# Kernel optimization log

Hardware: AMD Instinct MI355X
Metric: run time of the kernel (lower is better)

## Reference

```python
import jax, jax.numpy as jnp
import numpy as np


def _grid_sample_bilinear(img, grid):
    # img: [B,C,H,W]; grid: [B,Hg,Wg,2] normalized to [-1,1] (x,y), align_corners=False,
    # zero padding (torch F.grid_sample defaults).
    B, C, H, W = img.shape
    Hg, Wg = grid.shape[1], grid.shape[2]
    gx, gy = grid[..., 0], grid[..., 1]
    ix = (gx + 1.0) * (W * 0.5) - 0.5
    iy = (gy + 1.0) * (H * 0.5) - 0.5
    ix0 = jnp.floor(ix)
    iy0 = jnp.floor(iy)
    tx = (ix - ix0).reshape(B, 1, -1)
    ty = (iy - iy0).reshape(B, 1, -1)
    img_flat = img.reshape(B, C, H * W)

    def corner(xi, yi):
        valid = ((xi >= 0) & (xi < W) & (yi >= 0) & (yi < H)).reshape(B, 1, -1)
        xc = jnp.clip(xi, 0, W - 1).astype(jnp.int32)
        yc = jnp.clip(yi, 0, H - 1).astype(jnp.int32)
        idx = (yc * W + xc).reshape(B, -1)                      # [B, Hg*Wg]
        vals = jax.vmap(lambda f, i: f[:, i])(img_flat, idx)    # [B, C, Hg*Wg]
        return vals * valid

    v00 = corner(ix0, iy0)
    v01 = corner(ix0 + 1, iy0)
    v10 = corner(ix0, iy0 + 1)
    v11 = corner(ix0 + 1, iy0 + 1)
    out = (v00 * (1 - tx) * (1 - ty) + v01 * tx * (1 - ty)
           + v10 * (1 - tx) * ty + v11 * tx * ty)
    return out.reshape(B, C, Hg, Wg)


def setup_inputs() -> dict:
    key = jax.random.key(0)
    ks = jax.random.split(key, 8)
    B, C, RHO, WP = 32, 384, 25, 256
    HC, WC = 64, 64
    D = 2 * C  # 768, channels after polar/cart concat
    std = 0.02
    return {
        "polar_feat": jax.random.normal(ks[0], (B, C, RHO, WP), jnp.float32),
        "cart_feat": jax.random.normal(ks[1], (B, C, HC, WC), jnp.float32),
        "grid": jax.random.uniform(ks[2], (B, RHO, WP, 2), jnp.float32, -1.0, 1.0),
        "W1_0": jax.random.normal(ks[3], (D, 40), jnp.float32) * std,
        "b1_0": jnp.zeros((40,), jnp.float32),
        "W2_0": jax.random.normal(ks[4], (40, 1), jnp.float32) * std,
        "b2_0": jnp.zeros((1,), jnp.float32),
        "W1s": jax.random.normal(ks[5], (24, D + 1, 40), jnp.float32) * std,
        "b1s": jnp.zeros((24, 40), jnp.float32),
        "W2s": jax.random.normal(ks[6], (24, 40, 1), jnp.float32) * std,
        "b2s": jnp.zeros((24, 1), jnp.float32),
    }


def reference(polar_feat, cart_feat, grid, W1_0, b1_0, W2_0, b2_0, W1s, b1s, W2s, b2s):
    # Polar grid-sample fusion of cartesian features onto the polar grid.
    fe_cart_p = _grid_sample_bilinear(cart_feat, grid)              # [B,C,25,Wp]
    fe_cat_p = jnp.concatenate([polar_feat, fe_cart_p], axis=1)     # [B,768,25,Wp]
    # AdaptiveAvgPool2d((None,1)): mean over width.
    fe = jnp.mean(fe_cat_p, axis=3)                                 # [B,768,25]

    feats = jnp.transpose(fe, (2, 0, 1))                            # [25,B,768]
    gelu = lambda x: jax.nn.gelu(x, approximate=False)

    # Head 0: no recurrent input.
    h0 = gelu(feats[0] @ W1_0 + b1_0)
    out0 = h0 @ W2_0 + b2_0                                         # [B,1]

    # Heads 1..24: concat previous scalar output before first linear (fully_local=False).
    def step(out_prev, xs):
        feat, W1, b1, W2, b2 = xs
        x = jnp.concatenate([feat, out_prev], axis=-1)              # [B,769]
        h = gelu(x @ W1 + b1)
        o = h @ W2 + b2                                             # [B,1]
        return o, o

    _, outs = jax.lax.scan(step, out0, (feats[1:], W1s, b1s, W2s, b2s))
    out = jnp.concatenate([out0[None], outs], axis=0)               # [25,B,1]
    out = jnp.transpose(out[:, :, 0], (1, 0))                       # [B,25]
    return jnp.clip(out, 0.0, jnp.pi)
```

## Files before the change

kernel.cpp:

```cpp
#include <hip/hip_runtime.h>
#include <math.h>

#define B_    32
#define C_    384
#define RHO_  25
#define WP_   256
#define PIX_  4096
#define D_    768
#define HID_  40
#define NROWS (B_*C_*RHO_)
#define FE_N (RHO_*B_*D_)
#define POLARBLK 2048
#define PCH 8

typedef _Float16 half_t;
typedef __attribute__((ext_vector_type(8))) _Float16 half8;
typedef __attribute__((ext_vector_type(4))) float f32x4;

__device__ __forceinline__ float gelu_exact(float x) {
    return 0.5f * x * (1.f + erff(x * 0.70710678118654752f));
}

__global__ __launch_bounds__(256) void front_kernel(const float* __restrict__ polar,
        const float* __restrict__ grid,
        const float* __restrict__ W1_0, const float* __restrict__ W1s,
        half_t* __restrict__ Whi, half_t* __restrict__ Wlo,
        float* __restrict__ W1T, float* __restrict__ fe) {
    __shared__ float lb[PIX_];
    int tid = threadIdx.x;
    int bid = blockIdx.x;
    if (bid < POLARBLK) {
        int wid = bid * 4 + (tid >> 6);
        int lane = tid & 63;
        const int NW = POLARBLK * 4;
        for (int r0 = wid; r0 < NROWS; r0 += 4 * NW) {
            float s[4];
            #pragma unroll
            for (int k = 0; k < 4; ++k) {
                int r = r0 + k * NW;
                float4 v = (r < NROWS) ? ((const float4*)(polar + (size_t)r * WP_))[lane]
                                       : make_float4(0.f, 0.f, 0.f, 0.f);
                s[k] = v.x + v.y + v.z + v.w;
            }
            #pragma unroll
            for (int m = 32; m >= 1; m >>= 1) {
                #pragma unroll
                for (int k = 0; k < 4; ++k) s[k] += __shfl_xor(s[k], m, 64);
            }
            if (lane == 0) {
                #pragma unroll
                for (int k = 0; k < 4; ++k) {
                    int r = r0 + k * NW;
                    if (r < NROWS) {
                        int rho = r % RHO_, cch = (r / RHO_) % C_, bb = r / (RHO_ * C_);
                        fe[((size_t)(rho * B_ + bb)) * D_ + cch] = s[k] * (1.f / 256.f);
                    }
                }
            }
        }
    } else if (bid < POLARBLK + B_ * RHO_) {
        int bb = bid - POLARBLK;
        for (int i = tid; i < PIX_ / 4; i += 256) ((float4*)lb)[i] = make_float4(0.f, 0.f, 0.f, 0.f);
        __syncthreads();
        int pt = bb * WP_ + tid;
        float2 g = ((const float2*)grid)[pt];
        float ix = (g.x + 1.f) * 32.f - 0.5f;
        float iy = (g.y + 1.f) * 32.f - 0.5f;
        float x0f = floorf(ix), y0f = floorf(iy);
        float fx = ix - x0f, fy = iy - y0f;
        int x0 = (int)x0f, y0 = (int)y0f;
        const float s = 1.f / 256.f;
        if ((unsigned)x0 < 64u) {
            if ((unsigned)y0 < 64u)       atomicAdd(&lb[y0 * 64 + x0],       (1.f - fx) * (1.f - fy) * s);
            if ((unsigned)(y0 + 1) < 64u) atomicAdd(&lb[(y0 + 1) * 64 + x0], (1.f - fx) * fy * s);
        }
        if ((unsigned)(x0 + 1) < 64u) {
            if ((unsigned)y0 < 64u)       atomicAdd(&lb[y0 * 64 + x0 + 1],       fx * (1.f - fy) * s);
            if ((unsigned)(y0 + 1) < 64u) atomicAdd(&lb[(y0 + 1) * 64 + x0 + 1], fx * fy * s);
        }
        __syncthreads();
        int b = bb / RHO_, rho = bb % RHO_;
        half_t* wh = Whi + ((size_t)(b * 32 + rho)) * PIX_;
        half_t* wl = Wlo + ((size_t)(b * 32 + rho)) * PIX_;
        for (int i = tid; i < PIX_; i += 256) {
            float wv = lb[i];
            half_t h = (half_t)wv;
            wh[i] = h;
            wl[i] = (half_t)(wv - (float)h);
        }
    } else if (bid < POLARBLK + B_ * RHO_ + 25) {
        int i = bid - (POLARBLK + B_ * RHO_);
        const float* src = (i == 0) ? W1_0 : (W1s + (size_t)(i - 1) * 769 * HID_);
        float* dst = W1T + (size_t)i * HID_ * D_;
        for (int idx = tid; idx < HID_ * D_; idx += 256) {
            int j = idx / D_, c = idx % D_;
            dst[idx] = src[c * HID_ + j];
        }
    } else {
        int z = bid - (POLARBLK + B_ * RHO_ + 25);
        for (int i = tid; i < 16 * 96; i += 256) {
            int row = z * 16 + (i / 96), e = i % 96;
            ((float4*)fe)[(size_t)row * 192 + 96 + e] = make_float4(0.f, 0.f, 0.f, 0.f);
        }
    }
}

__global__ __launch_bounds__(256) void cart_mfma_kernel(const float* __restrict__ cart,
        const half_t* __restrict__ Whi, const half_t* __restrict__ Wlo,
        float* __restrict__ fe) {
    __shared__ float lds_out[1600];
    int tid = threadIdx.x;
    int bid = blockIdx.x;
    int b  = bid / (6 * PCH);
    int ct = (bid / PCH) % 6;
    int pc = bid % PCH;
    int w = tid >> 6, lane = tid & 63;
    int row16 = lane & 15, kg = lane >> 4;

    const float*  xrow = cart + ((size_t)b * C_ + ct * 64 + w * 16 + row16) * PIX_ + pc * 512 + kg * 8;
    const half_t* bh0 = Whi + ((size_t)(b * 32 + row16)) * PIX_ + pc * 512 + kg * 8;
    const half_t* bh1 = Whi + ((size_t)(b * 32 + 16 + row16)) * PIX_ + pc * 512 + kg * 8;
    const half_t* bl0 = Wlo + ((size_t)(b * 32 + row16)) * PIX_ + pc * 512 + kg * 8;
    const half_t* bl1 = Wlo + ((size_t)(b * 32 + 16 + row16)) * PIX_ + pc * 512 + kg * 8;

    f32x4 acc0 = {0.f, 0.f, 0.f, 0.f};
    f32x4 acc1 = {0.f, 0.f, 0.f, 0.f};

    float4 xa = *(const float4*)(xrow);
    float4 xb = *(const float4*)(xrow + 4);
    half8 nbh0 = *(const half8*)(bh0);
    half8 nbh1 = *(const half8*)(bh1);
    half8 nbl0 = *(const half8*)(bl0);
    half8 nbl1 = *(const half8*)(bl1);

    for (int t = 0; t < 16; ++t) {
        float4 cxa = xa, cxb = xb;
        half8 vbh0 = nbh0, vbh1 = nbh1, vbl0 = nbl0, vbl1 = nbl1;
        if (t < 15) {
            int off = (t + 1) * 32;
            xa = *(const float4*)(xrow + off);
            xb = *(const float4*)(xrow + off + 4);
            nbh0 = *(const half8*)(bh0 + off);
            nbh1 = *(const half8*)(bh1 + off);
            nbl0 = *(const half8*)(bl0 + off);
            nbl1 = *(const half8*)(bl1 + off);
        }
        float xs[8] = {cxa.x, cxa.y, cxa.z, cxa.w, cxb.x, cxb.y, cxb.z, cxb.w};
        half8 ah, al;
        #pragma unroll
        for (int i = 0; i < 8; ++i) {
            half_t h = (half_t)xs[i];
            ah[i] = h;
            al[i] = (half_t)(xs[i] - (float)h);
        }
        acc0 = __builtin_amdgcn_mfma_f32_16x16x32_f16(ah, vbh0, acc0, 0, 0, 0);
        acc0 = __builtin_amdgcn_mfma_f32_16x16x32_f16(ah, vbl0, acc0, 0, 0, 0);
        acc0 = __builtin_amdgcn_mfma_f32_16x16x32_f16(al, vbh0, acc0, 0, 0, 0);
        acc1 = __builtin_amdgcn_mfma_f32_16x16x32_f16(ah, vbh1, acc1, 0, 0, 0);
        acc1 = __builtin_amdgcn_mfma_f32_16x16x32_f16(ah, vbl1, acc1, 0, 0, 0);
        acc1 = __builtin_amdgcn_mfma_f32_16x16x32_f16(al, vbh1, acc1, 0, 0, 0);
    }

    #pragma unroll
    for (int r = 0; r < 4; ++r)
        lds_out[(lane & 15) * 64 + w * 16 + kg * 4 + r] = acc0[r];
    int rho1 = 16 + (lane & 15);
    if (rho1 < RHO_) {
        #pragma unroll
        for (int r = 0; r < 4; ++r)
            lds_out[rho1 * 64 + w * 16 + kg * 4 + r] = acc1[r];
    }
    __syncthreads();
    for (int oi = tid; oi < 1600; oi += 256) {
        int r = oi >> 6, cc = oi & 63;
        atomicAdd(&fe[((size_t)(r * B_ + b)) * D_ + 384 + ct * 64 + cc], lds_out[oi]);
    }
}

__global__ __launch_bounds__(256) void mlp_pre_kernel(const float* __restrict__ fe,
        const float* __restrict__ W1T, const float* __restrict__ b1_0,
        const float* __restrict__ b1s, float* __restrict__ G) {
    int lane = threadIdx.x & 63;
    int trip = blockIdx.x * 4 + (threadIdx.x >> 6);
    int jh = trip & 1;
    int pair = trip >> 1;
    int i = pair >> 5, b = pair & 31;
    const float4* f4p = (const float4*)(fe + (size_t)(i * B_ + b) * D_);
    float4 f0 = f4p[lane], f1 = f4p[lane + 64], f2 = f4p[lane + 128];
    int j0 = jh * 20;
    #pragma unroll 2
    for (int j = j0; j < j0 + 20; ++j) {
        const float4* w4p = (const float4*)(W1T + ((size_t)i * HID_ + j) * D_);
        float4 w0 = w4p[lane], w1 = w4p[lane + 64], w2 = w4p[lane + 128];
        float s = f0.x*w0.x + f0.y*w0.y + f0.z*w0.z + f0.w*w0.w
                + f1.x*w1.x + f1.y*w1.y + f1.z*w1.z + f1.w*w1.w
                + f2.x*w2.x + f2.y*w2.y + f2.z*w2.z + f2.w*w2.w;
        #pragma unroll
        for (int m = 32; m >= 1; m >>= 1) s += __shfl_xor(s, m, 64);
        if (lane == 0) {
            float bias = (i == 0) ? b1_0[j] : b1s[(i - 1) * HID_ + j];
            G[(size_t)(i * B_ + b) * HID_ + j] = s + bias;
        }
    }
}

__global__ __launch_bounds__(64) void mlp_seq_kernel(const float* __restrict__ G,
        const float* __restrict__ W1s, const float* __restrict__ W2_0,
        const float* __restrict__ b2_0, const float* __restrict__ W2s,
        const float* __restrict__ b2s, float* __restrict__ out) {
    int lane = threadIdx.x;
    int j2 = lane & 31, b = blockIdx.x * 2 + (lane >> 5);
    bool hi = (j2 < 8);
    float g1[25], g2[25], wl1[25], wl2[25], w2a[25], w2b[25], bsc[25];
    #pragma unroll
    for (int i = 0; i < 25; ++i) {
        g1[i] = G[(size_t)(i * B_ + b) * HID_ + j2];
        g2[i] = hi ? G[(size_t)(i * B_ + b) * HID_ + 32 + j2] : 0.f;
    }
    wl1[0] = 0.f; wl2[0] = 0.f;
    w2a[0] = W2_0[j2]; w2b[0] = hi ? W2_0[32 + j2] : 0.f; bsc[0] = b2_0[0];
    #pragma unroll
    for (int i = 1; i < 25; ++i) {
        size_t base = ((size_t)(i - 1) * 769 + 768) * HID_;
        wl1[i] = W1s[base + j2];
        wl2[i] = hi ? W1s[base + 32 + j2] : 0.f;
        w2a[i] = W2s[(i - 1) * HID_ + j2];
        w2b[i] = hi ? W2s[(i - 1) * HID_ + 32 + j2] : 0.f;
        bsc[i] = b2s[i - 1];
    }
    float op = 0.f;
    #pragma unroll
    for (int i = 0; i < 25; ++i) {
        float x1 = g1[i] + op * wl1[i];
        float x2 = g2[i] + op * wl2[i];
        float p = gelu_exact(x1) * w2a[i] + gelu_exact(x2) * w2b[i];
        #pragma unroll
        for (int m = 16; m >= 1; m >>= 1) p += __shfl_xor(p, m, 64);
        float o = p + bsc[i];
        op = o;
        if (j2 == 0) out[b * 25 + i] = fminf(fmaxf(o, 0.f), 3.14159265358979323846f);
    }
}

extern "C" void kernel_launch(void* const* d_in, const int* in_sizes, int n_in,
                              void* d_out, int out_size, void* d_ws, size_t ws_size,
                              hipStream_t stream) {
    const float* polar = (const float*)d_in[0];
    const float* cart  = (const float*)d_in[1];
    const float* grid  = (const float*)d_in[2];
    const float* W1_0  = (const float*)d_in[3];
    const float* b1_0  = (const float*)d_in[4];
    const float* W2_0  = (const float*)d_in[5];
    const float* b2_0  = (const float*)d_in[6];
    const float* W1s   = (const float*)d_in[7];
    const float* b1s   = (const float*)d_in[8];
    const float* W2s   = (const float*)d_in[9];
    const float* b2s   = (const float*)d_in[10];
    float* out = (float*)d_out;

    half_t* Whi = (half_t*)d_ws;
    half_t* Wlo = Whi + (size_t)B_ * 32 * PIX_;
    float* fe   = (float*)(Wlo + (size_t)B_ * 32 * PIX_);
    float* G    = fe + (size_t)FE_N;
    float* W1T  = G + (size_t)RHO_ * B_ * HID_;

    front_kernel<<<POLARBLK + B_ * RHO_ + 25 + 50, 256, 0, stream>>>(polar, grid, W1_0, W1s, Whi, Wlo, W1T, fe);
    cart_mfma_kernel<<<B_ * 6 * PCH, 256, 0, stream>>>(cart, Whi, Wlo, fe);
    mlp_pre_kernel<<<(RHO_ * B_ * 2) / 4, 256, 0, stream>>>(fe, W1T, b1_0, b1s, G);
    mlp_seq_kernel<<<B_ / 2, 64, 0, stream>>>(G, W1s, W2_0, b2_0, W2s, b2s, out);
}
```

Baseline: 198.3 us.

## Stage cart rows through per-wave LDS double buffer for coalesced loads

The cart-feature GEMM kernel no longer has each lane read its own strided 32-byte pieces of global memory. Each wave now loads 64-column tiles of its 16 rows with row-contiguous float4 reads, writes them into a padded, double-buffered per-wave LDS area, and reads the MFMA A fragments back from LDS. Weight fragments are prefetched two K-steps ahead in registers. This is meant to improve global load coalescing and hide latency, at the cost of about 34KB of LDS per block (lower occupancy), more registers, and LDS traffic. It relies on wave-local ordering with no barrier between the LDS writes and reads.

Result: faster. 175.4 us (-11.5%).

```diff
diff --git a/kernel.cpp b/kernel.cpp
--- a/kernel.cpp
+++ b/kernel.cpp
@@ -108,7 +108,7 @@
 __global__ __launch_bounds__(256) void cart_mfma_kernel(const float* __restrict__ cart,
         const half_t* __restrict__ Whi, const half_t* __restrict__ Wlo,
         float* __restrict__ fe) {
-    __shared__ float lds_out[1600];
+    __shared__ float smem[8704];
     int tid = threadIdx.x;
     int bid = blockIdx.x;
     int b  = bid / (6 * PCH);
@@ -117,63 +117,102 @@
     int w = tid >> 6, lane = tid & 63;
     int row16 = lane & 15, kg = lane >> 4;
 
-    const float*  xrow = cart + ((size_t)b * C_ + ct * 64 + w * 16 + row16) * PIX_ + pc * 512 + kg * 8;
+    const float* xgbase = cart + ((size_t)b * C_ + ct * 64 + w * 16) * PIX_ + pc * 512;
     const half_t* bh0 = Whi + ((size_t)(b * 32 + row16)) * PIX_ + pc * 512 + kg * 8;
-    const half_t* bh1 = Whi + ((size_t)(b * 32 + 16 + row16)) * PIX_ + pc * 512 + kg * 8;
+    const half_t* bh1 = bh0 + (size_t)16 * PIX_;
     const half_t* bl0 = Wlo + ((size_t)(b * 32 + row16)) * PIX_ + pc * 512 + kg * 8;
-    const half_t* bl1 = Wlo + ((size_t)(b * 32 + 16 + row16)) * PIX_ + pc * 512 + kg * 8;
+    const half_t* bl1 = bl0 + (size_t)16 * PIX_;
+
+    float* xl = smem + w * 2176;
+    int srow = lane >> 4;
+    int scol = (lane & 15) * 4;
 
     f32x4 acc0 = {0.f, 0.f, 0.f, 0.f};
     f32x4 acc1 = {0.f, 0.f, 0.f, 0.f};
-
-    float4 xa = *(const float4*)(xrow);
-    float4 xb = *(const float4*)(xrow + 4);
-    half8 nbh0 = *(const half8*)(bh0);
-    half8 nbh1 = *(const half8*)(bh1);
-    half8 nbl0 = *(const half8*)(bl0);
-    half8 nbl1 = *(const half8*)(bl1);
-
-    for (int t = 0; t < 16; ++t) {
-        float4 cxa = xa, cxb = xb;
-        half8 vbh0 = nbh0, vbh1 = nbh1, vbl0 = nbl0, vbl1 = nbl1;
-        if (t < 15) {
-            int off = (t + 1) * 32;
-            xa = *(const float4*)(xrow + off);
-            xb = *(const float4*)(xrow + off + 4);
-            nbh0 = *(const half8*)(bh0 + off);
-            nbh1 = *(const half8*)(bh1 + off);
-            nbl0 = *(const half8*)(bl0 + off);
-            nbl1 = *(const half8*)(bl1 + off);
-        }
-        float xs[8] = {cxa.x, cxa.y, cxa.z, cxa.w, cxb.x, cxb.y, cxb.z, cxb.w};
-        half8 ah, al;
+    float4 sreg[4];
+    half8 wf[2][8];
+
+    #pragma unroll
+    for (int i = 0; i < 4; ++i)
+        sreg[i] = *(const float4*)(xgbase + (size_t)(srow + 4 * i) * PIX_ + scol);
+    #pragma unroll
+    for (int ks = 0; ks < 2; ++ks) {
+        wf[0][ks * 4 + 0] = *(const half8*)(bh0 + ks * 32);
+        wf[0][ks * 4 + 1] = *(const half8*)(bh1 + ks * 32);
+        wf[0][ks * 4 + 2] = *(const half8*)(bl0 + ks * 32);
+        wf[0][ks * 4 + 3] = *(const half8*)(bl1 + ks * 32);
+    }
+    #pragma unroll
+    for (int i = 0; i < 4; ++i)
+        *(float4*)(&xl[(srow + 4 * i) * 68 + scol]) = sreg[i];
+    #pragma unroll
+    for (int i = 0; i < 4; ++i)
+        sreg[i] = *(const float4*)(xgbase + (size_t)(srow + 4 * i) * PIX_ + 64 + scol);
+    #pragma unroll
+    for (int ks = 0; ks < 2; ++ks) {
+        wf[1][ks * 4 + 0] = *(const half8*)(bh0 + 64 + ks * 32);
+        wf[1][ks * 4 + 1] = *(const half8*)(bh1 + 64 + ks * 32);
+        wf[1][ks * 4 + 2] = *(const half8*)(bl0 + 64 + ks * 32);
+        wf[1][ks * 4 + 3] = *(const half8*)(bl1 + 64 + ks * 32);
+    }
+
+    #pragma unroll
+    for (int t = 0; t < 8; ++t) {
+        const int cb = t & 1;
+        const float* xb = xl + cb * 1088;
         #pragma unroll
-        for (int i = 0; i < 8; ++i) {
-            half_t h = (half_t)xs[i];
-            ah[i] = h;
-            al[i] = (half_t)(xs[i] - (float)h);
-        }
-        acc0 = __builtin_amdgcn_mfma_f32_16x16x32_f16(ah, vbh0, acc0, 0, 0, 0);
-        acc0 = __builtin_amdgcn_mfma_f32_16x16x32_f16(ah, vbl0, acc0, 0, 0, 0);
-        acc0 = __builtin_amdgcn_mfma_f32_16x16x32_f16(al, vbh0, acc0, 0, 0, 0);
-        acc1 = __builtin_amdgcn_mfma_f32_16x16x32_f16(ah, vbh1, acc1, 0, 0, 0);
-        acc1 = __builtin_amdgcn_mfma_f32_16x16x32_f16(ah, vbl1, acc1, 0, 0, 0);
-        acc1 = __builtin_amdgcn_mfma_f32_16x16x32_f16(al, vbh1, acc1, 0, 0, 0);
-    }
-
+        for (int ks = 0; ks < 2; ++ks) {
+            float4 xa = *(const float4*)(xb + row16 * 68 + ks * 32 + kg * 8);
+            float4 xc = *(const float4*)(xb + row16 * 68 + ks * 32 + kg * 8 + 4);
+            float xs[8] = {xa.x, xa.y, xa.z, xa.w, xc.x, xc.y, xc.z, xc.w};
+            half8 ah, al;
+            #pragma unroll
+            for (int i = 0; i < 8; ++i) {
+                half_t h = (half_t)xs[i];
+                ah[i] = h;
+                al[i] = (half_t)(xs[i] - (float)h);
+            }
+            acc0 = __builtin_amdgcn_mfma_f32_16x16x32_f16(ah, wf[cb][ks * 4 + 0], acc0, 0, 0, 0);
+            acc0 = __builtin_amdgcn_mfma_f32_16x16x32_f16(ah, wf[cb][ks * 4 + 2], acc0, 0, 0, 0);
+            acc0 = __builtin_amdgcn_mfma_f32_16x16x32_f16(al, wf[cb][ks * 4 + 0], acc0, 0, 0, 0);
+            acc1 = __builtin_amdgcn_mfma_f32_16x16x32_f16(ah, wf[cb][ks * 4 + 1], acc1, 0, 0, 0);
+            acc1 = __builtin_amdgcn_mfma_f32_16x16x32_f16(ah, wf[cb][ks * 4 + 3], acc1, 0, 0, 0);
+            acc1 = __builtin_amdgcn_mfma_f32_16x16x32_f16(al, wf[cb][ks * 4 + 1], acc1, 0, 0, 0);
+        }
+        if (t < 7) {
+            #pragma unroll
+            for (int i = 0; i < 4; ++i)
+                *(float4*)(&xl[(cb ^ 1) * 1088 + (srow + 4 * i) * 68 + scol]) = sreg[i];
+            if (t < 6) {
+                int off = (t + 2) * 64;
+                #pragma unroll
+                for (int i = 0; i < 4; ++i)
+                    sreg[i] = *(const float4*)(xgbase + (size_t)(srow + 4 * i) * PIX_ + off + scol);
+                #pragma unroll
+                for (int ks = 0; ks < 2; ++ks) {
+                    wf[cb][ks * 4 + 0] = *(const half8*)(bh0 + off + ks * 32);
+                    wf[cb][ks * 4 + 1] = *(const half8*)(bh1 + off + ks * 32);
+                    wf[cb][ks * 4 + 2] = *(const half8*)(bl0 + off + ks * 32);
+                    wf[cb][ks * 4 + 3] = *(const half8*)(bl1 + off + ks * 32);
+                }
+            }
+        }
+    }
+
+    __syncthreads();
     #pragma unroll
     for (int r = 0; r < 4; ++r)
-        lds_out[(lane & 15) * 64 + w * 16 + kg * 4 + r] = acc0[r];
-    int rho1 = 16 + (lane & 15);
+        smem[row16 * 64 + w * 16 + kg * 4 + r] = acc0[r];
+    int rho1 = 16 + row16;
     if (rho1 < RHO_) {
         #pragma unroll
         for (int r = 0; r < 4; ++r)
-            lds_out[rho1 * 64 + w * 16 + kg * 4 + r] = acc1[r];
+            smem[rho1 * 64 + w * 16 + kg * 4 + r] = acc1[r];
     }
     __syncthreads();
     for (int oi = tid; oi < 1600; oi += 256) {
         int r = oi >> 6, cc = oi & 63;
-        atomicAdd(&fe[((size_t)(r * B_ + b)) * D_ + 384 + ct * 64 + cc], lds_out[oi]);
+        atomicAdd(&fe[((size_t)(r * B_ + b)) * D_ + 384 + ct * 64 + cc], smem[oi]);
     }
 }
 
```
